# Performance work log

Measured on AMD Instinct MI355X. Metric: run time of the kernel, lower is better.

Reference implementation:

```python
import jax, jax.numpy as jnp
import numpy as np

NUM_USERS = 100000
NUM_ITEMS = 50000
EMBED_DIM = 64
NNZ = 4_000_000
BATCH = 4096
N_LAYERS = 3
WEIGHT_DECAY = 1e-4


def setup_inputs() -> dict:
    key = jax.random.key(0)
    ks = jax.random.split(key, 8)
    N = NUM_USERS + NUM_ITEMS
    user_emb = 0.1 * jax.random.normal(ks[0], (NUM_USERS, EMBED_DIM), dtype=jnp.float32)
    item_emb = 0.1 * jax.random.normal(ks[1], (NUM_ITEMS, EMBED_DIM), dtype=jnp.float32)
    graph_rows = jax.random.randint(ks[2], (NNZ,), 0, N, dtype=jnp.int32)
    graph_cols = jax.random.randint(ks[3], (NNZ,), 0, N, dtype=jnp.int32)
    # normalized-adjacency-like small positive values
    graph_vals = 0.05 * jax.random.uniform(ks[4], (NNZ,), dtype=jnp.float32)
    users = jax.random.randint(ks[5], (BATCH,), 0, NUM_USERS, dtype=jnp.int32)
    positive_items = jax.random.randint(ks[6], (BATCH,), 0, NUM_ITEMS, dtype=jnp.int32)
    negative_items = jax.random.randint(ks[7], (BATCH,), 0, NUM_ITEMS, dtype=jnp.int32)
    return {
        "user_emb": user_emb,
        "item_emb": item_emb,
        "graph_rows": graph_rows,
        "graph_cols": graph_cols,
        "graph_vals": graph_vals,
        "users": users,
        "positive_items": positive_items,
        "negative_items": negative_items,
    }


def _spmm(rows, cols, vals, x, n):
    # sparse (n,n) @ x[n,d] via gather + segment_sum
    return jax.ops.segment_sum(vals[:, None] * x[cols], rows, num_segments=n)


def reference(user_emb, item_emb, graph_rows, graph_cols, graph_vals,
              users, positive_items, negative_items):
    N = user_emb.shape[0] + item_emb.shape[0]
    all_e = jnp.concatenate([user_emb, item_emb], axis=0)  # [N, D]
    acc = all_e
    cur = all_e
    for _ in range(N_LAYERS):
        cur = _spmm(graph_rows, graph_cols, graph_vals, cur, N)
        acc = acc + cur
    light_out = acc / jnp.float32(N_LAYERS + 1)  # mean over stacked layers

    nu = user_emb.shape[0]
    u_e = light_out[users]
    p_e = light_out[nu + positive_items]
    n_e = light_out[nu + negative_items]

    u_o = user_emb[users]
    p_o = item_emb[positive_items]
    n_o = item_emb[negative_items]

    B = users.shape[0]
    regular = 0.5 * (jnp.sum(u_o ** 2) + jnp.sum(p_o ** 2) + jnp.sum(n_o ** 2)) / jnp.float32(B)
    pos_s = jnp.sum(u_e * p_e, axis=1)
    neg_s = jnp.sum(u_e * n_e, axis=1)
    loss = jnp.mean(jax.nn.softplus(neg_s - pos_s)) + WEIGHT_DECAY * regular
    return loss
```

## Files before the change

kernel.cpp:

```cpp
#include <hip/hip_runtime.h>
#include <math.h>

#define NU 100000
#define NI 50000
#define NT 150000
#define D  64
#define NNZ_ 4000000
#define BATCH_ 4096
#define WDECAY 1e-4f

#define BROWS 2048
#define NBKT 74
#define BCAP 57344
#define CURS 16
#define EPB 16
#define BATCH_E (256 * EPB)
#define NBLK_A ((NNZ_ + BATCH_E - 1) / BATCH_E)
#define NBLO 512

static __device__ __forceinline__ float bf2f(ushort u) {
    return __uint_as_float(((unsigned int)u) << 16);
}
static __device__ __forceinline__ ushort f2bf(float f) {
    unsigned int u = __float_as_uint(f);
    u += 0x7FFF + ((u >> 16) & 1);
    return (ushort)(u >> 16);
}

__global__ void init_kernel(const float* __restrict__ ue, const float* __restrict__ ie,
                            ushort* __restrict__ cur0) {
    int i = blockIdx.x * blockDim.x + threadIdx.x;
    const int total4 = NT * D / 4;
    if (i >= total4) return;
    const int usz4 = NU * D / 4;
    float4 v = (i < usz4) ? ((const float4*)ue)[i] : ((const float4*)ie)[i - usz4];
    ushort4 o;
    o.x = f2bf(v.x); o.y = f2bf(v.y); o.z = f2bf(v.z); o.w = f2bf(v.w);
    ((ushort4*)cur0)[i] = o;
}

__global__ void binA_kernel(const int* __restrict__ rows, const int* __restrict__ cols,
                            const float* __restrict__ vals,
                            int* __restrict__ cursor, int2* __restrict__ binned) {
    __shared__ int cnt[NBKT];
    __shared__ int gbase[NBKT];
    int tid = threadIdx.x;
    int b0 = blockIdx.x * BATCH_E;
    if (tid < NBKT) cnt[tid] = 0;
    __syncthreads();
    int pack[EPB];
    #pragma unroll
    for (int k = 0; k < EPB; ++k) {
        int i = b0 + k * 256 + tid;
        if (i < NNZ_) {
            int r = rows[i];
            int b = r >> 11;
            int rk = atomicAdd(&cnt[b], 1);
            pack[k] = (r & (BROWS - 1)) | (b << 11) | (rk << 18);
        } else pack[k] = -1;
    }
    __syncthreads();
    if (tid < NBKT) {
        int c = cnt[tid];
        gbase[tid] = c ? atomicAdd(&cursor[tid * CURS], c) : 0;
    }
    __syncthreads();
    #pragma unroll
    for (int k = 0; k < EPB; ++k) {
        int pk = pack[k];
        if (pk >= 0) {
            int i  = b0 + k * 256 + tid;
            int rl = pk & (BROWS - 1);
            int b  = (pk >> 11) & 127;
            int rk = pk >> 18;
            int2 e;
            e.x = rl | (cols[i] << 11);
            e.y = __float_as_int(vals[i]);
            binned[(size_t)b * BCAP + gbase[b] + rk] = e;
        }
    }
}

__global__ void bscan_kernel(const int* __restrict__ cursor, int* __restrict__ bbase,
                             int* __restrict__ rowptr) {
    __shared__ int s[128];
    int t = threadIdx.x;
    int v = (t < NBKT) ? cursor[t * CURS] : 0;
    s[t] = v; __syncthreads();
    for (int off = 1; off < 128; off <<= 1) {
        int x = (t >= off) ? s[t - off] : 0;
        __syncthreads();
        s[t] += x;
        __syncthreads();
    }
    if (t < NBKT) bbase[t] = s[t] - v;
    if (t == 0) rowptr[NT] = NNZ_;
}

__global__ void binB_kernel(const int2* __restrict__ binned, const int* __restrict__ cursor,
                            const int* __restrict__ bbase,
                            int2* __restrict__ colval, int* __restrict__ rowptr) {
    __shared__ int cnt[BROWS];
    __shared__ int sc[1024];
    __shared__ int offs[BROWS];
    int b   = blockIdx.x;
    int tid = threadIdx.x;
    int cb  = cursor[b * CURS];
    int base = bbase[b];
    const int2* eb = binned + (size_t)b * BCAP;
    cnt[tid] = 0; cnt[tid + 1024] = 0;
    __syncthreads();
    for (int i = tid; i < cb; i += 1024)
        atomicAdd(&cnt[eb[i].x & (BROWS - 1)], 1);
    __syncthreads();
    int v0 = cnt[2 * tid], v1 = cnt[2 * tid + 1];
    sc[tid] = v0 + v1;
    __syncthreads();
    for (int off = 1; off < 1024; off <<= 1) {
        int x = (tid >= off) ? sc[tid - off] : 0;
        __syncthreads();
        sc[tid] += x;
        __syncthreads();
    }
    int pbase = sc[tid] - (v0 + v1);
    offs[2 * tid]     = pbase;
    offs[2 * tid + 1] = pbase + v0;
    int row0 = b * BROWS + 2 * tid;
    if (row0 < NT)     rowptr[row0]     = base + pbase;
    if (row0 + 1 < NT) rowptr[row0 + 1] = base + pbase + v0;
    __syncthreads();
    for (int i = tid; i < cb; i += 1024) {
        int2 e = eb[i];
        int rl = e.x & (BROWS - 1);
        int p  = base + atomicAdd(&offs[rl], 1);
        int2 cv; cv.x = e.x >> 11; cv.y = e.y;
        colval[p] = cv;
    }
}

static __device__ __forceinline__ void row_core(const int* __restrict__ rowptr,
                                                const int2* __restrict__ colval,
                                                const ushort* __restrict__ x,
                                                int r, int lane,
                                                float& s0, float& s1, float& s2, float& s3) {
    int q  = lane >> 4;
    int ql = lane & 15;
    int beg = rowptr[r], end = rowptr[r + 1];
    s0 = s1 = s2 = s3 = 0.f;
    for (int base = beg; base < end; base += 64) {
        int m = end - base; if (m > 64) m = 64;
        int idx = base + lane; if (idx > NNZ_ - 1) idx = NNZ_ - 1;
        int2 cv = colval[idx];
        int nq = (m + 3) >> 2;
        #pragma unroll 8
        for (int j = 0; j < nq; ++j) {
            int e = 4 * j + q;
            int   c = __shfl(cv.x, e);
            float v = __int_as_float(__shfl(cv.y, e));
            if (e >= m) v = 0.f;
            ushort4 xv = *(const ushort4*)(x + (size_t)c * D + ql * 4);
            s0 += v * bf2f(xv.x); s1 += v * bf2f(xv.y);
            s2 += v * bf2f(xv.z); s3 += v * bf2f(xv.w);
        }
    }
    s0 += __shfl_xor(s0, 16); s0 += __shfl_xor(s0, 32);
    s1 += __shfl_xor(s1, 16); s1 += __shfl_xor(s1, 32);
    s2 += __shfl_xor(s2, 16); s2 += __shfl_xor(s2, 32);
    s3 += __shfl_xor(s3, 16); s3 += __shfl_xor(s3, 32);
}

__global__ void spmm_kernel(const int* __restrict__ rowptr, const int2* __restrict__ colval,
                            const ushort* __restrict__ x, ushort* __restrict__ y) {
    int gtid = blockIdx.x * blockDim.x + threadIdx.x;
    int r    = gtid >> 6;
    int lane = threadIdx.x & 63;
    if (r >= NT) return;
    float s0, s1, s2, s3;
    row_core(rowptr, colval, x, r, lane, s0, s1, s2, s3);
    if ((lane >> 4) == 0) {
        int ql = lane & 15;
        ushort4 o;
        o.x = f2bf(s0); o.y = f2bf(s1); o.z = f2bf(s2); o.w = f2bf(s3);
        *(ushort4*)(y + (size_t)r * D + ql * 4) = o;
    }
}

__global__ void walk_kernel(const ushort* __restrict__ o2,
                            const int* __restrict__ rowptr, const int2* __restrict__ colval,
                            const int* __restrict__ users, const int* __restrict__ pos,
                            const int* __restrict__ neg, float* __restrict__ wbuf) {
    int gtid = blockIdx.x * blockDim.x + threadIdx.x;
    int task = gtid >> 6;
    int lane = threadIdx.x & 63;
    if (task >= 3 * BATCH_) return;
    int role = task >> 12;
    int b    = task & (BATCH_ - 1);
    int r = (role == 0) ? users[b] : (role == 1) ? NU + pos[b] : NU + neg[b];
    float s0, s1, s2, s3;
    row_core(rowptr, colval, o2, r, lane, s0, s1, s2, s3);
    if ((lane >> 4) == 0) {
        int ql = lane & 15;
        float4 o; o.x = s0; o.y = s1; o.z = s2; o.w = s3;
        *(float4*)(wbuf + (size_t)task * D + ql * 4) = o;
    }
}

__global__ void loss_kernel(const float* __restrict__ ue, const float* __restrict__ ie,
                            const ushort* __restrict__ o1, const ushort* __restrict__ o2,
                            const float* __restrict__ wbuf,
                            const int* __restrict__ users, const int* __restrict__ pos,
                            const int* __restrict__ neg, float* __restrict__ pbuf) {
    __shared__ float ssp[4];
    __shared__ float srg[4];
    int tid  = threadIdx.x;
    int wv   = tid >> 6;
    int lane = tid & 63;
    int wid  = blockIdx.x * 4 + wv;
    const int nw = NBLO * 4;
    float sp_acc = 0.f, rg_acc = 0.f;
    for (int b = wid; b < BATCH_; b += nw) {
        int u = users[b], p = pos[b], n = neg[b];
        int ru = u, rp = NU + p, rn = NU + n;
        float uo = ue[(size_t)u * D + lane];
        float po = ie[(size_t)p * D + lane];
        float no = ie[(size_t)n * D + lane];
        float lu = uo + bf2f(o1[(size_t)ru * D + lane]) + bf2f(o2[(size_t)ru * D + lane])
                      + wbuf[(size_t)(0 * BATCH_ + b) * D + lane];
        float lp = po + bf2f(o1[(size_t)rp * D + lane]) + bf2f(o2[(size_t)rp * D + lane])
                      + wbuf[(size_t)(1 * BATCH_ + b) * D + lane];
        float ln_ = no + bf2f(o1[(size_t)rn * D + lane]) + bf2f(o2[(size_t)rn * D + lane])
                      + wbuf[(size_t)(2 * BATCH_ + b) * D + lane];
        float ps = lu * lp;
        float ns = lu * ln_;
        float rg = uo * uo + po * po + no * no;
        #pragma unroll
        for (int off = 32; off > 0; off >>= 1) {
            ps += __shfl_down(ps, off);
            ns += __shfl_down(ns, off);
            rg += __shfl_down(rg, off);
        }
        if (lane == 0) {
            float diff = (ns - ps) * (1.0f / 16.0f);
            float sp = diff > 0.f ? diff + log1pf(expf(-diff)) : log1pf(expf(diff));
            sp_acc += sp;
            rg_acc += rg;
        }
    }
    if (lane == 0) { ssp[wv] = sp_acc; srg[wv] = rg_acc; }
    __syncthreads();
    if (tid == 0) {
        pbuf[blockIdx.x]        = ssp[0] + ssp[1] + ssp[2] + ssp[3];
        pbuf[NBLO + blockIdx.x] = srg[0] + srg[1] + srg[2] + srg[3];
    }
}

__global__ void finalize_kernel(const float* __restrict__ pbuf, float* __restrict__ out) {
    __shared__ float s1[NBLO];
    __shared__ float s2[NBLO];
    int t = threadIdx.x;
    s1[t] = pbuf[t];
    s2[t] = pbuf[NBLO + t];
    __syncthreads();
    for (int off = NBLO / 2; off > 0; off >>= 1) {
        if (t < off) { s1[t] += s1[t + off]; s2[t] += s2[t + off]; }
        __syncthreads();
    }
    if (t == 0)
        out[0] = s1[0] / (float)BATCH_ + WDECAY * 0.5f * s2[0] / (float)BATCH_;
}

extern "C" void kernel_launch(void* const* d_in, const int* in_sizes, int n_in,
                              void* d_out, int out_size, void* d_ws, size_t ws_size,
                              hipStream_t stream) {
    const float* user_emb = (const float*)d_in[0];
    const float* item_emb = (const float*)d_in[1];
    const int*   g_rows   = (const int*)d_in[2];
    const int*   g_cols   = (const int*)d_in[3];
    const float* g_vals   = (const float*)d_in[4];
    const int*   users    = (const int*)d_in[5];
    const int*   pos      = (const int*)d_in[6];
    const int*   neg      = (const int*)d_in[7];
    float* out = (float*)d_out;

    const size_t TABH = (size_t)NT * D * 2;
    char* ws = (char*)d_ws;
    ushort* cur0   = (ushort*)(ws);
    ushort* o1     = (ushort*)(ws + TABH);
    ushort* o2     = (ushort*)(ws + 2 * TABH);
    int2*   colval = (int2*)  (ws + 3 * TABH);
    int2*   binned = (int2*)  (ws + 3 * TABH + (size_t)NNZ_ * 8);
    char*   p      = ws + 3 * TABH + (size_t)NNZ_ * 8 + (size_t)NBKT * BCAP * 8;
    int*    rowptr = (int*)(p);      p += ((size_t)(NT + 1) * 4 + 255) / 256 * 256;
    int*    cursor = (int*)(p);      p += (size_t)NBKT * CURS * 4;
    int*    bbase  = (int*)(p);      p += 1024;
    float*  pbuf   = (float*)(p);    p += 2 * NBLO * 4;
    float*  wbuf   = (float*)(p);

    hipMemsetAsync(cursor, 0, (size_t)NBKT * CURS * 4, stream);
    init_kernel<<<(NT * D / 4 + 255) / 256, 256, 0, stream>>>(user_emb, item_emb, cur0);

    binA_kernel<<<NBLK_A, 256, 0, stream>>>(g_rows, g_cols, g_vals, cursor, binned);
    bscan_kernel<<<1, 128, 0, stream>>>(cursor, bbase, rowptr);
    binB_kernel<<<NBKT, 1024, 0, stream>>>(binned, cursor, bbase, colval, rowptr);

    const int SPMM_BLOCKS = (NT + 3) / 4;
    spmm_kernel<<<SPMM_BLOCKS, 256, 0, stream>>>(rowptr, colval, cur0, o1);
    spmm_kernel<<<SPMM_BLOCKS, 256, 0, stream>>>(rowptr, colval, o1, o2);

    walk_kernel<<<(3 * BATCH_ + 3) / 4, 256, 0, stream>>>(o2, rowptr, colval,
                                                          users, pos, neg, wbuf);
    loss_kernel<<<NBLO, 256, 0, stream>>>(user_emb, item_emb, o1, o2, wbuf,
                                          users, pos, neg, pbuf);
    finalize_kernel<<<1, NBLO, 0, stream>>>(pbuf, out);
}
```

Baseline: 469.5 us.

## Shrink CSR build buckets, widen SpMM row gathers, add nontemporal loads

The row-binning buckets shrink from 2048 to 512 rows, which gives 293 buckets instead of 74 so the binB CSR build runs across more blocks. The SpMM row core now has 8-lane groups each load 16 bytes (8 bf16 values) per neighbor instead of 4 values, which halves the shuffle and gather iterations per row. Nontemporal loads are used on streaming inputs, and the workspace is rearranged so wbuf and pbuf alias the binned buffer. The main risks are the smaller bucket capacity (15360) overflowing under skewed row distributions, and higher register pressure in the gather loop.

Result: no change. 472.1 us (+0.6%).

```diff
diff --git a/kernel.cpp b/kernel.cpp
--- a/kernel.cpp
+++ b/kernel.cpp
@@ -9,9 +9,9 @@
 #define BATCH_ 4096
 #define WDECAY 1e-4f
 
-#define BROWS 2048
-#define NBKT 74
-#define BCAP 57344
+#define BROWS 512
+#define NBKT 293
+#define BCAP 15360
 #define CURS 16
 #define EPB 16
 #define BATCH_E (256 * EPB)
@@ -20,6 +20,12 @@
 
 static __device__ __forceinline__ float bf2f(ushort u) {
     return __uint_as_float(((unsigned int)u) << 16);
+}
+static __device__ __forceinline__ float bflo(unsigned int u) {
+    return __uint_as_float(u << 16);
+}
+static __device__ __forceinline__ float bfhi(unsigned int u) {
+    return __uint_as_float(u & 0xffff0000u);
 }
 static __device__ __forceinline__ ushort f2bf(float f) {
     unsigned int u = __float_as_uint(f);
@@ -46,23 +52,23 @@
     __shared__ int gbase[NBKT];
     int tid = threadIdx.x;
     int b0 = blockIdx.x * BATCH_E;
-    if (tid < NBKT) cnt[tid] = 0;
+    for (int t = tid; t < NBKT; t += 256) cnt[t] = 0;
     __syncthreads();
     int pack[EPB];
     #pragma unroll
     for (int k = 0; k < EPB; ++k) {
         int i = b0 + k * 256 + tid;
         if (i < NNZ_) {
-            int r = rows[i];
-            int b = r >> 11;
+            int r = __builtin_nontemporal_load(rows + i);
+            int b = r >> 9;
             int rk = atomicAdd(&cnt[b], 1);
-            pack[k] = (r & (BROWS - 1)) | (b << 11) | (rk << 18);
+            pack[k] = (r & (BROWS - 1)) | (b << 9) | (rk << 18);
         } else pack[k] = -1;
     }
     __syncthreads();
-    if (tid < NBKT) {
-        int c = cnt[tid];
-        gbase[tid] = c ? atomicAdd(&cursor[tid * CURS], c) : 0;
+    for (int t = tid; t < NBKT; t += 256) {
+        int c = cnt[t];
+        gbase[t] = c ? atomicAdd(&cursor[t * CURS], c) : 0;
     }
     __syncthreads();
     #pragma unroll
@@ -71,11 +77,11 @@
         if (pk >= 0) {
             int i  = b0 + k * 256 + tid;
             int rl = pk & (BROWS - 1);
-            int b  = (pk >> 11) & 127;
+            int b  = (pk >> 9) & 511;
             int rk = pk >> 18;
             int2 e;
-            e.x = rl | (cols[i] << 11);
-            e.y = __float_as_int(vals[i]);
+            e.x = rl | (__builtin_nontemporal_load(cols + i) << 9);
+            e.y = __float_as_int(__builtin_nontemporal_load(vals + i));
             binned[(size_t)b * BCAP + gbase[b] + rk] = e;
         }
     }
@@ -83,11 +89,11 @@
 
 __global__ void bscan_kernel(const int* __restrict__ cursor, int* __restrict__ bbase,
                              int* __restrict__ rowptr) {
-    __shared__ int s[128];
+    __shared__ int s[512];
     int t = threadIdx.x;
     int v = (t < NBKT) ? cursor[t * CURS] : 0;
     s[t] = v; __syncthreads();
-    for (int off = 1; off < 128; off <<= 1) {
+    for (int off = 1; off < 512; off <<= 1) {
         int x = (t >= off) ? s[t - off] : 0;
         __syncthreads();
         s[t] += x;
@@ -101,39 +107,43 @@
                             const int* __restrict__ bbase,
                             int2* __restrict__ colval, int* __restrict__ rowptr) {
     __shared__ int cnt[BROWS];
-    __shared__ int sc[1024];
+    __shared__ int sc[BROWS];
     __shared__ int offs[BROWS];
     int b   = blockIdx.x;
     int tid = threadIdx.x;
     int cb  = cursor[b * CURS];
     int base = bbase[b];
-    const int2* eb = binned + (size_t)b * BCAP;
-    cnt[tid] = 0; cnt[tid + 1024] = 0;
-    __syncthreads();
-    for (int i = tid; i < cb; i += 1024)
-        atomicAdd(&cnt[eb[i].x & (BROWS - 1)], 1);
-    __syncthreads();
-    int v0 = cnt[2 * tid], v1 = cnt[2 * tid + 1];
-    sc[tid] = v0 + v1;
-    __syncthreads();
-    for (int off = 1; off < 1024; off <<= 1) {
-        int x = (tid >= off) ? sc[tid - off] : 0;
-        __syncthreads();
-        sc[tid] += x;
-        __syncthreads();
-    }
-    int pbase = sc[tid] - (v0 + v1);
-    offs[2 * tid]     = pbase;
-    offs[2 * tid + 1] = pbase + v0;
-    int row0 = b * BROWS + 2 * tid;
-    if (row0 < NT)     rowptr[row0]     = base + pbase;
-    if (row0 + 1 < NT) rowptr[row0 + 1] = base + pbase + v0;
+    const unsigned long long* eb8 = (const unsigned long long*)(binned + (size_t)b * BCAP);
+    if (tid < BROWS) cnt[tid] = 0;
     __syncthreads();
     for (int i = tid; i < cb; i += 1024) {
-        int2 e = eb[i];
-        int rl = e.x & (BROWS - 1);
+        unsigned long long e = __builtin_nontemporal_load(eb8 + i);
+        atomicAdd(&cnt[(int)e & (BROWS - 1)], 1);
+    }
+    __syncthreads();
+    int v = 0;
+    if (tid < BROWS) { v = cnt[tid]; sc[tid] = v; }
+    __syncthreads();
+    for (int off = 1; off < BROWS; off <<= 1) {
+        int x = 0;
+        if (tid < BROWS && tid >= off) x = sc[tid - off];
+        __syncthreads();
+        if (tid < BROWS) sc[tid] += x;
+        __syncthreads();
+    }
+    if (tid < BROWS) {
+        int excl = sc[tid] - v;
+        offs[tid] = excl;
+        int row = b * BROWS + tid;
+        if (row < NT) rowptr[row] = base + excl;
+    }
+    __syncthreads();
+    for (int i = tid; i < cb; i += 1024) {
+        unsigned long long e = __builtin_nontemporal_load(eb8 + i);
+        int ex = (int)e;
+        int rl = ex & (BROWS - 1);
         int p  = base + atomicAdd(&offs[rl], 1);
-        int2 cv; cv.x = e.x >> 11; cv.y = e.y;
+        int2 cv; cv.x = ex >> 9; cv.y = (int)(e >> 32);
         colval[p] = cv;
     }
 }
@@ -142,31 +152,40 @@
                                                 const int2* __restrict__ colval,
                                                 const ushort* __restrict__ x,
                                                 int r, int lane,
-                                                float& s0, float& s1, float& s2, float& s3) {
-    int q  = lane >> 4;
-    int ql = lane & 15;
+                                                float& s0, float& s1, float& s2, float& s3,
+                                                float& s4, float& s5, float& s6, float& s7) {
+    int g  = lane >> 3;
+    int gl = lane & 7;
     int beg = rowptr[r], end = rowptr[r + 1];
-    s0 = s1 = s2 = s3 = 0.f;
+    s0 = s1 = s2 = s3 = s4 = s5 = s6 = s7 = 0.f;
+    const unsigned long long* cv8 = (const unsigned long long*)colval;
     for (int base = beg; base < end; base += 64) {
         int m = end - base; if (m > 64) m = 64;
         int idx = base + lane; if (idx > NNZ_ - 1) idx = NNZ_ - 1;
-        int2 cv = colval[idx];
-        int nq = (m + 3) >> 2;
+        unsigned long long e8 = __builtin_nontemporal_load(cv8 + idx);
+        int cvx = (int)e8;
+        int cvy = (int)(e8 >> 32);
+        int ng = (m + 7) >> 3;
         #pragma unroll 8
-        for (int j = 0; j < nq; ++j) {
-            int e = 4 * j + q;
-            int   c = __shfl(cv.x, e);
-            float v = __int_as_float(__shfl(cv.y, e));
+        for (int j = 0; j < ng; ++j) {
+            int e = 8 * j + g;
+            int   c = __shfl(cvx, e);
+            float v = __int_as_float(__shfl(cvy, e));
             if (e >= m) v = 0.f;
-            ushort4 xv = *(const ushort4*)(x + (size_t)c * D + ql * 4);
-            s0 += v * bf2f(xv.x); s1 += v * bf2f(xv.y);
-            s2 += v * bf2f(xv.z); s3 += v * bf2f(xv.w);
+            uint4 w = *(const uint4*)(x + (size_t)c * D + gl * 8);
+            s0 += v * bflo(w.x); s1 += v * bfhi(w.x);
+            s2 += v * bflo(w.y); s3 += v * bfhi(w.y);
+            s4 += v * bflo(w.z); s5 += v * bfhi(w.z);
+            s6 += v * bflo(w.w); s7 += v * bfhi(w.w);
         }
     }
-    s0 += __shfl_xor(s0, 16); s0 += __shfl_xor(s0, 32);
-    s1 += __shfl_xor(s1, 16); s1 += __shfl_xor(s1, 32);
-    s2 += __shfl_xor(s2, 16); s2 += __shfl_xor(s2, 32);
-    s3 += __shfl_xor(s3, 16); s3 += __shfl_xor(s3, 32);
+    #pragma unroll
+    for (int off = 8; off < 64; off <<= 1) {
+        s0 += __shfl_xor(s0, off); s1 += __shfl_xor(s1, off);
+        s2 += __shfl_xor(s2, off); s3 += __shfl_xor(s3, off);
+        s4 += __shfl_xor(s4, off); s5 += __shfl_xor(s5, off);
+        s6 += __shfl_xor(s6, off); s7 += __shfl_xor(s7, off);
+    }
 }
 
 __global__ void spmm_kernel(const int* __restrict__ rowptr, const int2* __restrict__ colval,
@@ -175,13 +194,15 @@
     int r    = gtid >> 6;
     int lane = threadIdx.x & 63;
     if (r >= NT) return;
-    float s0, s1, s2, s3;
-    row_core(rowptr, colval, x, r, lane, s0, s1, s2, s3);
-    if ((lane >> 4) == 0) {
-        int ql = lane & 15;
-        ushort4 o;
-        o.x = f2bf(s0); o.y = f2bf(s1); o.z = f2bf(s2); o.w = f2bf(s3);
-        *(ushort4*)(y + (size_t)r * D + ql * 4) = o;
+    float s0, s1, s2, s3, s4, s5, s6, s7;
+    row_core(rowptr, colval, x, r, lane, s0, s1, s2, s3, s4, s5, s6, s7);
+    if (lane < 8) {
+        uint4 o;
+        o.x = (unsigned)f2bf(s0) | ((unsigned)f2bf(s1) << 16);
+        o.y = (unsigned)f2bf(s2) | ((unsigned)f2bf(s3) << 16);
+        o.z = (unsigned)f2bf(s4) | ((unsigned)f2bf(s5) << 16);
+        o.w = (unsigned)f2bf(s6) | ((unsigned)f2bf(s7) << 16);
+        *(uint4*)(y + (size_t)r * D + lane * 8) = o;
     }
 }
 
@@ -196,12 +217,14 @@
     int role = task >> 12;
     int b    = task & (BATCH_ - 1);
     int r = (role == 0) ? users[b] : (role == 1) ? NU + pos[b] : NU + neg[b];
-    float s0, s1, s2, s3;
-    row_core(rowptr, colval, o2, r, lane, s0, s1, s2, s3);
-    if ((lane >> 4) == 0) {
-        int ql = lane & 15;
-        float4 o; o.x = s0; o.y = s1; o.z = s2; o.w = s3;
-        *(float4*)(wbuf + (size_t)task * D + ql * 4) = o;
+    float s0, s1, s2, s3, s4, s5, s6, s7;
+    row_core(rowptr, colval, o2, r, lane, s0, s1, s2, s3, s4, s5, s6, s7);
+    if (lane < 8) {
+        float4 a; a.x = s0; a.y = s1; a.z = s2; a.w = s3;
+        float4 c; c.x = s4; c.y = s5; c.z = s6; c.w = s7;
+        float* dst = wbuf + (size_t)task * D + lane * 8;
+        *(float4*)dst = a;
+        *(float4*)(dst + 4) = c;
     }
 }
 
@@ -288,19 +311,20 @@
     ushort* o1     = (ushort*)(ws + TABH);
     ushort* o2     = (ushort*)(ws + 2 * TABH);
     int2*   colval = (int2*)  (ws + 3 * TABH);
-    int2*   binned = (int2*)  (ws + 3 * TABH + (size_t)NNZ_ * 8);
-    char*   p      = ws + 3 * TABH + (size_t)NNZ_ * 8 + (size_t)NBKT * BCAP * 8;
+    char*   bpt    = ws + 3 * TABH + (size_t)NNZ_ * 8;
+    int2*   binned = (int2*)  (bpt);
+    float*  wbuf   = (float*)(bpt);
+    float*  pbuf   = (float*)(bpt + 4 * 1024 * 1024);
+    char*   p      = bpt + (size_t)NBKT * BCAP * 8;
     int*    rowptr = (int*)(p);      p += ((size_t)(NT + 1) * 4 + 255) / 256 * 256;
-    int*    cursor = (int*)(p);      p += (size_t)NBKT * CURS * 4;
-    int*    bbase  = (int*)(p);      p += 1024;
-    float*  pbuf   = (float*)(p);    p += 2 * NBLO * 4;
-    float*  wbuf   = (float*)(p);
+    int*    cursor = (int*)(p);      p += (size_t)NBKT * CURS * 4 + 256;
+    int*    bbase  = (int*)(p);      p += 2048;
 
     hipMemsetAsync(cursor, 0, (size_t)NBKT * CURS * 4, stream);
     init_kernel<<<(NT * D / 4 + 255) / 256, 256, 0, stream>>>(user_emb, item_emb, cur0);
 
     binA_kernel<<<NBLK_A, 256, 0, stream>>>(g_rows, g_cols, g_vals, cursor, binned);
-    bscan_kernel<<<1, 128, 0, stream>>>(cursor, bbase, rowptr);
+    bscan_kernel<<<1, 512, 0, stream>>>(cursor, bbase, rowptr);
     binB_kernel<<<NBKT, 1024, 0, stream>>>(binned, cursor, bbase, colval, rowptr);
 
     const int SPMM_BLOCKS = (NT + 3) / 4;
```
